# Optimization experiments

Hardware: AMD Instinct MI355X
Metric: run time of the kernel (lower is better)

Reference implementation:

```python
import jax, jax.numpy as jnp
import numpy as np

MODES = 32
WIDTH = 64


def crelu(z):
    # split-complex ReLU (torch.relu is undefined on complex; this is the standard fix)
    return jax.nn.relu(z.real) + 1j * jax.nn.relu(z.imag)


def _linear_params(key, fan_in, fan_out):
    k1, k2 = jax.random.split(key)
    s = 1.0 / np.sqrt(fan_in)
    W = jax.random.uniform(k1, (fan_out, fan_in), minval=-s, maxval=s, dtype=jnp.float32)
    b = jax.random.uniform(k2, (fan_out,), minval=-s, maxval=s, dtype=jnp.float32)
    return W, b


def setup_inputs() -> dict:
    key = jax.random.key(0)
    ks = jax.random.split(key, 8)
    B, G = 32768, 512
    H0, H1, H2 = 1024, 512, 64  # hidden_layers; H2 == WIDTH
    FD = 128                    # field_dim
    geometry_input = jax.random.normal(ks[0], (B, G), dtype=jnp.float32)
    W_in, b_in = _linear_params(ks[1], G, H0)
    W_h1, b_h1 = _linear_params(ks[2], H0, H1)
    W_h2, b_h2 = _linear_params(ks[3], H1, H2)
    w0 = jax.random.normal(ks[4], (MODES, WIDTH), dtype=jnp.float32)
    w1 = jax.random.normal(ks[5], (MODES, WIDTH), dtype=jnp.float32)
    lin1_W, lin1_b = _linear_params(ks[6], WIDTH, WIDTH)
    k7a, k7b = jax.random.split(ks[7])
    lin2_W, lin2_b = _linear_params(k7a, WIDTH, WIDTH)
    W_out, b_out = _linear_params(k7b, H2, FD)
    return dict(geometry_input=geometry_input, W_in=W_in, b_in=b_in,
                W_h1=W_h1, b_h1=b_h1, W_h2=W_h2, b_h2=b_h2,
                w0=w0, w1=w1, lin1_W=lin1_W, lin1_b=lin1_b,
                lin2_W=lin2_W, lin2_b=lin2_b, W_out=W_out, b_out=b_out)


def reference(geometry_input, W_in, b_in, W_h1, b_h1, W_h2, b_h2,
              w0, w1, lin1_W, lin1_b, lin2_W, lin2_b, W_out, b_out):
    # MLP encoder: [B, G] -> [B, 64]
    x = jax.nn.relu(geometry_input @ W_in.T + b_in)
    x = jax.nn.relu(x @ W_h1.T + b_h1)
    x = jax.nn.relu(x @ W_h2.T + b_h2)
    # FNO block
    xh = jnp.fft.fftn(x)  # fftn over ALL axes, as in torch code -> complex64 [B, 64]
    phase = jnp.exp(1j * 2.0 * jnp.pi * jnp.arange(MODES) / MODES).astype(jnp.complex64)
    y = xh[:, None, :] * w0  # per-mode lift: [B, MODES, WIDTH]
    y = crelu(y)
    y = y * phase[None, :, None]  # diagonal L mode-multiply
    y = jnp.einsum('bmw,mw->bw', y, w1.astype(y.dtype))  # collapse modes -> [B, WIDTH]
    y = crelu(y @ lin1_W.T + lin1_b)  # real weights on complex acts
    y = y @ lin2_W.T + lin2_b
    y = jnp.fft.ifftn(y)  # [B, 64] complex
    out = y @ W_out.T + b_out  # [B, field_dim] complex
    return out
```

## Files before the change

### kernel.cpp

```cpp
#include <hip/hip_runtime.h>
#include <hip/hip_bf16.h>


#define PI2F 6.28318530717958647692f

typedef __attribute__((ext_vector_type(8))) short short8;
typedef __attribute__((ext_vector_type(4))) float f32x4;

__device__ __forceinline__ unsigned short f2bf(float f) {
  unsigned int u = __float_as_uint(f);
  u += 0x7fff + ((u >> 16) & 1);
  return (unsigned short)(u >> 16);
}
__device__ __forceinline__ unsigned int pack_bf16x2(float a, float b) {
  return (unsigned int)f2bf(a) | ((unsigned int)f2bf(b) << 16);
}

__device__ __forceinline__ void gl2lds16(const void* gptr, const void* lptr) {
  __builtin_amdgcn_global_load_lds(
      (const __attribute__((address_space(1))) unsigned int*)(unsigned long long)gptr,
      (__attribute__((address_space(3))) unsigned int*)(unsigned int)(unsigned long long)lptr,
      16, 0, 0);
}

__global__ __launch_bounds__(256) void conv_all(
    const float* __restrict__ geom, const float* __restrict__ Win,
    const float* __restrict__ Wh1, const float* __restrict__ Wh2,
    unsigned short* __restrict__ dg, unsigned short* __restrict__ dw,
    unsigned short* __restrict__ d1, unsigned short* __restrict__ d2)
{
  int i = blockIdx.x * 256 + threadIdx.x;
  const float* s; unsigned short* d; int off;
  if (i < 4194304)      { s = geom; d = dg; off = i; }
  else if (i < 4325376) { s = Win;  d = dw; off = i - 4194304; }
  else if (i < 4456448) { s = Wh1;  d = d1; off = i - 4325376; }
  else if (i < 4464640) { s = Wh2;  d = d2; off = i - 4456448; }
  else return;
  float4 v = ((const float4*)s)[off];
  uint2 p;
  p.x = pack_bf16x2(v.x, v.y);
  p.y = pack_bf16x2(v.z, v.w);
  ((uint2*)d)[off] = p;
}

template<int NBLOG, typename OUT>
__global__ __launch_bounds__(512, 1) void gemm_pipe(
    const unsigned short* __restrict__ A, const unsigned short* __restrict__ Bw,
    const float* __restrict__ bias, OUT* __restrict__ C, int N, int K)
{
  constexpr int BM = 128, BN = 256, BK = 64;
  constexpr int ASZ = BM * BK;
  constexpr int BSZ = BN * BK;
  constexpr int BUF = ASZ + BSZ;
  __shared__ __align__(16) unsigned short lds[3 * BUF];

  const int nwg = gridDim.x;
  const int cpx = nwg >> 3;
  const int orig = blockIdx.x;
  const int wg = (orig & 7) * cpx + (orig >> 3);
  const int mb = wg >> NBLOG;
  const int nb = wg & ((1 << NBLOG) - 1);
  const size_t m0 = (size_t)mb * BM;
  const size_t n0 = (size_t)nb * BN;

  const int tid = threadIdx.x;
  const int lane = tid & 63;
  const int wv = tid >> 6;
  const int q = lane >> 4, lr = lane & 15;
  const int x7 = lr & 7;
  const int wm = (wv >> 2) * 64;
  const int wn = (wv & 3) * 64;
  f32x4 acc[4][4] = {};

  auto STAGE = [&](int r, int kk) {
    unsigned short* dA = lds + r * BUF;
    #pragma unroll
    for (int u = 0; u < 6; ++u) {
      int e = wv * 6 + u;
      int isA = (e < 16) ? 1 : 0;
      int e2 = isA ? e : e - 16;
      int pc = e2 * 64 + lane;
      int row = pc >> 3, col = pc & 7;
      int lc = col ^ (row & 7);
      const unsigned short* src = isA ? A : Bw;
      size_t rb = isA ? m0 : n0;
      unsigned short* dst = dA + (isA ? 0 : ASZ) + e2 * 512;
      gl2lds16(src + (rb + row) * (size_t)K + kk + lc * 8, dst);
    }
  };

  const int nt = K / BK;
  STAGE(0, 0);
  STAGE(1, BK);
  asm volatile("s_waitcnt vmcnt(6)" ::: "memory");
  __builtin_amdgcn_s_barrier();

  int r0 = 0;
  for (int t = 0; t < nt; ++t) {
    const unsigned short* sA = lds + r0 * BUF;
    const unsigned short* sB = sA + ASZ;
    const bool st = (t + 2) < nt;
    const int r2 = (r0 >= 1) ? (r0 - 1) : 2;
    const int kk2 = (t + 2) * BK;

    short8 af[4][2], bfr[4][2];
    #pragma unroll
    for (int i = 0; i < 4; ++i)
      #pragma unroll
      for (int t2 = 0; t2 < 2; ++t2)
        af[i][t2] = *(const short8*)(sA + (wm + i * 16 + lr) * 64 + (((t2 << 2) | q) ^ x7) * 8);
    #pragma unroll
    for (int j = 0; j < 4; ++j)
      #pragma unroll
      for (int t2 = 0; t2 < 2; ++t2)
        bfr[j][t2] = *(const short8*)(sB + (wn + j * 16 + lr) * 64 + (((t2 << 2) | q) ^ x7) * 8);
    if (st) STAGE(r2, kk2);
    __builtin_amdgcn_s_setprio(1);
    #pragma unroll
    for (int i = 0; i < 4; ++i)
      #pragma unroll
      for (int j = 0; j < 4; ++j)
        #pragma unroll
        for (int t2 = 0; t2 < 2; ++t2)
          acc[i][j] = __builtin_amdgcn_mfma_f32_16x16x32_bf16(af[i][t2], bfr[j][t2], acc[i][j], 0, 0, 0);
    __builtin_amdgcn_s_setprio(0);

    asm volatile("s_waitcnt lgkmcnt(0)" ::: "memory");
    if (st) { asm volatile("s_waitcnt vmcnt(6)" ::: "memory"); }
    else    { asm volatile("s_waitcnt vmcnt(0)" ::: "memory"); }
    __builtin_amdgcn_s_barrier();
    r0 = (r0 + 1 >= 3) ? 0 : r0 + 1;
  }

  #pragma unroll
  for (int i = 0; i < 4; ++i)
    #pragma unroll
    for (int j = 0; j < 4; ++j) {
      size_t col = n0 + wn + j * 16 + lr;
      float bv = bias[col];
      #pragma unroll
      for (int r = 0; r < 4; ++r) {
        size_t row = m0 + wm + i * 16 + q * 4 + r;
        float v = acc[i][j][r] + bv;
        v = v > 0.f ? v : 0.f;
        if (sizeof(OUT) == 2) ((unsigned short*)C)[row * N + col] = f2bf(v);
        else                  ((float*)C)[row * N + col] = v;
      }
    }
}

__global__ __launch_bounds__(256) void gemm3_dft(
    const unsigned short* __restrict__ A, const unsigned short* __restrict__ Bw,
    const float* __restrict__ bias, float2* __restrict__ S0, int K)
{
  constexpr int BM = 128, BN = 64, BK = 64;
  __shared__ __align__(16) unsigned short lA[BM * BK];
  __shared__ __align__(16) unsigned short lB[BN * BK];
  __shared__ __align__(16) float xt[128][68];
  __shared__ float2 tw[64];
  const int tid = threadIdx.x;
  const int lane = tid & 63;
  const int wv = tid >> 6;
  const int q = lane >> 4, lr = lane & 15;
  const int x7 = lr & 7;
  const int wm = (wv >> 1) * 64;
  const int wn = (wv & 1) * 32;
  const size_t m0 = (size_t)blockIdx.x * BM;
  f32x4 acc[4][2] = {};
  constexpr int A_PW = (BM * BK / 512) / 4;
  constexpr int B_PW = (BN * BK / 512) / 4;

  if (tid < 64) {
    float sn, cs; sincosf(-PI2F * (float)tid / 64.f, &sn, &cs);
    tw[tid] = make_float2(cs, sn);
  }

  for (int k0 = 0; k0 < K; k0 += BK) {
    __syncthreads();
    #pragma unroll
    for (int s = 0; s < A_PW; ++s) {
      int instr = wv * A_PW + s;
      int pc = instr * 64 + lane;
      int row = pc >> 3, col = pc & 7;
      int lc = col ^ (row & 7);
      gl2lds16(A + (m0 + row) * (size_t)K + k0 + lc * 8, lA + instr * 512);
    }
    #pragma unroll
    for (int s = 0; s < B_PW; ++s) {
      int instr = wv * B_PW + s;
      int pc = instr * 64 + lane;
      int row = pc >> 3, col = pc & 7;
      int lc = col ^ (row & 7);
      gl2lds16(Bw + (size_t)row * K + k0 + lc * 8, lB + instr * 512);
    }
    __syncthreads();
    #pragma unroll
    for (int t = 0; t < 2; ++t) {
      short8 af[4], bfr[2];
      #pragma unroll
      for (int i = 0; i < 4; ++i) {
        int r = wm + i * 16 + lr;
        af[i] = *(const short8*)(lA + r * 64 + (((t << 2) | q) ^ x7) * 8);
      }
      #pragma unroll
      for (int j = 0; j < 2; ++j) {
        int r = wn + j * 16 + lr;
        bfr[j] = *(const short8*)(lB + r * 64 + (((t << 2) | q) ^ x7) * 8);
      }
      #pragma unroll
      for (int i = 0; i < 4; ++i)
        #pragma unroll
        for (int j = 0; j < 2; ++j)
          acc[i][j] = __builtin_amdgcn_mfma_f32_16x16x32_bf16(af[i], bfr[j], acc[i][j], 0, 0, 0);
    }
  }

  __syncthreads();
  #pragma unroll
  for (int i = 0; i < 4; ++i)
    #pragma unroll
    for (int j = 0; j < 2; ++j) {
      int col = wn + j * 16 + lr;
      float bv = bias[col];
      #pragma unroll
      for (int r = 0; r < 4; ++r) {
        int rowl = wm + i * 16 + q * 4 + r;
        float v = acc[i][j][r] + bv;
        xt[rowl][col] = v > 0.f ? v : 0.f;
      }
    }
  __syncthreads();

  const int k = tid & 63, rg = tid >> 6;
  #pragma unroll 1
  for (int half = 0; half < 2; ++half) {
    const int rb = rg * 32 + half * 16;
    float2 dacc[16] = {};
    #pragma unroll 1
    for (int w4 = 0; w4 < 16; ++w4) {
      int w = 4 * w4;
      int kw = k * w;
      float2 t0 = tw[kw & 63];
      float2 t1 = tw[(kw + k) & 63];
      float2 t2 = tw[(kw + 2 * k) & 63];
      float2 t3 = tw[(kw + 3 * k) & 63];
      #pragma unroll
      for (int r = 0; r < 16; ++r) {
        float4 xv = *(const float4*)(&xt[rb + r][w]);
        dacc[r].x += xv.x * t0.x + xv.y * t1.x + xv.z * t2.x + xv.w * t3.x;
        dacc[r].y += xv.x * t0.y + xv.y * t1.y + xv.z * t2.y + xv.w * t3.y;
      }
    }
    #pragma unroll
    for (int r = 0; r < 16; ++r)
      S0[(m0 + rb + r) * 64 + k] = dacc[r];
  }
}

__global__ __launch_bounds__(256) void precompute(
    const float* __restrict__ w0, const float* __restrict__ w1,
    const float* __restrict__ l2W, const float* __restrict__ l2b,
    float2* __restrict__ Ap, float2* __restrict__ Am,
    float2* __restrict__ Qt, float2* __restrict__ b2c)
{
  const int t = threadIdx.x;
  const int blk = blockIdx.x;
  if (blk == 0) {
    if (t < 64) {
      float apx = 0, apy = 0, amx = 0, amy = 0;
      for (int m = 0; m < 32; ++m) {
        float s0 = w0[m * 64 + t];
        float cf = w1[m * 64 + t] * s0;
        float sn, cs; sincosf(PI2F * (float)m / 32.f, &sn, &cs);
        if (s0 > 0.f)      { apx += cs * cf; apy += sn * cf; }
        else if (s0 < 0.f) { amx += cs * cf; amy += sn * cf; }
      }
      Ap[t] = make_float2(apx, apy);
      Am[t] = make_float2(amx, amy);
      float bx = 0, by = 0;
      for (int k = 0; k < 64; ++k) {
        float sn, cs; sincosf(PI2F * (float)((t * k) & 63) / 64.f, &sn, &cs);
        float lb = l2b[k] * (1.f / 64.f);
        bx += cs * lb; by += sn * lb;
      }
      b2c[t] = make_float2(bx, by);
    }
  } else {
    int e = (blk - 1) * 256 + t;
    int j = e >> 6, w = e & 63;
    float qx = 0, qy = 0;
    for (int k = 0; k < 64; ++k) {
      float sn, cs; sincosf(PI2F * (float)((j * k) & 63) / 64.f, &sn, &cs);
      float lw = l2W[k * 64 + w] * (1.f / 64.f);
      qx += cs * lw; qy += sn * lw;
    }
    Qt[w * 64 + j] = make_float2(qx, qy);
  }
}

template<int SIGN>
__global__ __launch_bounds__(256) void fft_stage1(
    const float2* __restrict__ Xin, float2* __restrict__ T)
{
  __shared__ __align__(16) float2 tile[128 * 34];
  __shared__ float2 tw16s[16];
  const int blk = blockIdx.x;
  const int b2 = blk >> 1, wh = (blk & 1) * 32;
  const int t = threadIdx.x;
  #pragma unroll
  for (int it = 0; it < 8; ++it) {
    int idx = it * 256 + t;
    int b1 = idx >> 4, wi = (idx & 15) * 2;
    float4 v = *(const float4*)&Xin[((size_t)(b1 * 256 + b2)) * 64 + wh + wi];
    *(float4*)&tile[b1 * 34 + wi] = v;
  }
  if (t < 16) {
    float sn, cs; sincosf(SIGN * PI2F * (float)t / 16.f, &sn, &cs);
    tw16s[t] = make_float2(cs, sn);
  }
  __syncthreads();
  float2 twr[16];
  #pragma unroll
  for (int j = 0; j < 16; ++j) twr[j] = tw16s[j];

  {
    const int n2a = t >> 5, w = t & 31;
    float2 d[16];
    #pragma unroll
    for (int n1 = 0; n1 < 16; ++n1)
      d[n1] = tile[(8 * n1 + n2a) * 34 + w];
    float2 y[16];
    #pragma unroll
    for (int k = 0; k < 16; ++k) {
      float2 a = d[0];
      #pragma unroll
      for (int n1 = 1; n1 < 16; ++n1) {
        float2 tv = twr[(n1 * k) & 15];
        a.x += d[n1].x * tv.x - d[n1].y * tv.y;
        a.y += d[n1].x * tv.y + d[n1].y * tv.x;
      }
      y[k] = a;
    }
    float sstep, cstep;
    sincosf(SIGN * PI2F * (float)n2a / 128.f, &sstep, &cstep);
    float2 rot = make_float2(1.f, 0.f);
    #pragma unroll
    for (int k = 0; k < 16; ++k) {
      float2 a = y[k];
      y[k] = make_float2(a.x * rot.x - a.y * rot.y, a.x * rot.y + a.y * rot.x);
      float nrx = rot.x * cstep - rot.y * sstep;
      rot.y = rot.x * sstep + rot.y * cstep;
      rot.x = nrx;
    }
    __syncthreads();
    #pragma unroll
    for (int k = 0; k < 16; ++k)
      tile[(n2a * 16 + k) * 34 + w] = y[k];
  }
  __syncthreads();

  const int wB = t & 31, qB = t >> 5;
  float sstep, cstep;
  sincosf(SIGN * PI2F * (float)(16 * b2) / 32768.f, &sstep, &cstep);
  #pragma unroll
  for (int h = 0; h < 2; ++h) {
    const int k1p = qB + 8 * h;
    float2 d[8];
    #pragma unroll
    for (int n2 = 0; n2 < 8; ++n2)
      d[n2] = tile[(n2 * 16 + k1p) * 34 + wB];
    float2 acc[8];
    #pragma unroll
    for (int k2p = 0; k2p < 8; ++k2p) {
      float2 a = d[0];
      #pragma unroll
      for (int n2 = 1; n2 < 8; ++n2) {
        float2 tv = twr[(2 * n2 * k2p) & 15];
        a.x += d[n2].x * tv.x - d[n2].y * tv.y;
        a.y += d[n2].x * tv.y + d[n2].y * tv.x;
      }
      acc[k2p] = a;
    }
    float sb, cb;
    sincosf(SIGN * PI2F * (float)(b2 * k1p) / 32768.f, &sb, &cb);
    float2 rot = make_float2(cb, sb);
    #pragma unroll
    for (int k2p = 0; k2p < 8; ++k2p) {
      int k1 = k1p + 16 * k2p;
      float2 a = acc[k2p];
      T[((size_t)k1 * 256 + b2) * 64 + wh + wB] =
          make_float2(a.x * rot.x - a.y * rot.y, a.x * rot.y + a.y * rot.x);
      float nrx = rot.x * cstep - rot.y * sstep;
      rot.y = rot.x * sstep + rot.y * cstep;
      rot.x = nrx;
    }
  }
}

template<int SIGN, bool SCALE>
__global__ __launch_bounds__(256) void fft_stage2(
    const float2* __restrict__ T, float2* __restrict__ X)
{
  __shared__ __align__(16) float2 tile[256 * 18];
  __shared__ float2 tw16s[16];
  const int blk = blockIdx.x;
  const int k1 = blk >> 2, wq = (blk & 3) * 16;
  const int t = threadIdx.x;
  #pragma unroll
  for (int it = 0; it < 8; ++it) {
    int idx = it * 256 + t;
    int r2 = idx >> 3, wi = (idx & 7) * 2;
    float4 v = *(const float4*)&T[((size_t)k1 * 256 + r2) * 64 + wq + wi];
    *(float4*)&tile[r2 * 18 + wi] = v;
  }
  if (t < 16) {
    float sn, cs; sincosf(SIGN * PI2F * (float)t / 16.f, &sn, &cs);
    tw16s[t] = make_float2(cs, sn);
  }
  __syncthreads();
  float2 twr[16];
  #pragma unroll
  for (int j = 0; j < 16; ++j) twr[j] = tw16s[j];

  {
    const int n2a = t >> 4, w = t & 15;
    float2 d[16];
    #pragma unroll
    for (int n1 = 0; n1 < 16; ++n1)
      d[n1] = tile[(16 * n1 + n2a) * 18 + w];
    float2 y[16];
    #pragma unroll
    for (int k = 0; k < 16; ++k) {
      float2 a = d[0];
      #pragma unroll
      for (int n1 = 1; n1 < 16; ++n1) {
        float2 tv = twr[(n1 * k) & 15];
        a.x += d[n1].x * tv.x - d[n1].y * tv.y;
        a.y += d[n1].x * tv.y + d[n1].y * tv.x;
      }
      y[k] = a;
    }
    float sstep, cstep;
    sincosf(SIGN * PI2F * (float)n2a / 256.f, &sstep, &cstep);
    float2 rot = make_float2(1.f, 0.f);
    #pragma unroll
    for (int k = 0; k < 16; ++k) {
      float2 a = y[k];
      y[k] = make_float2(a.x * rot.x - a.y * rot.y, a.x * rot.y + a.y * rot.x);
      float nrx = rot.x * cstep - rot.y * sstep;
      rot.y = rot.x * sstep + rot.y * cstep;
      rot.x = nrx;
    }
    __syncthreads();
    #pragma unroll
    for (int k = 0; k < 16; ++k)
      tile[(n2a * 16 + k) * 18 + w] = y[k];
  }
  __syncthreads();

  const int k1pb = t >> 4, wB = t & 15;
  float2 d[16];
  #pragma unroll
  for (int n2 = 0; n2 < 16; ++n2)
    d[n2] = tile[(n2 * 16 + k1pb) * 18 + wB];
  const float sc = SCALE ? (1.f / 32768.f) : 1.f;
  #pragma unroll
  for (int k2p = 0; k2p < 16; ++k2p) {
    float2 a = d[0];
    #pragma unroll
    for (int n2 = 1; n2 < 16; ++n2) {
      float2 tv = twr[(n2 * k2p) & 15];
      a.x += d[n2].x * tv.x - d[n2].y * tv.y;
      a.y += d[n2].x * tv.y + d[n2].y * tv.x;
    }
    int k2 = k1pb + 16 * k2p;
    size_t row = (size_t)(k1 + 128 * k2);
    X[row * 64 + wq + wB] = make_float2(a.x * sc, a.y * sc);
  }
}

__global__ __launch_bounds__(256) void pw_lin(
    const float2* __restrict__ xh,
    const float2* __restrict__ Ap, const float2* __restrict__ Am,
    const float* __restrict__ l1W, const float* __restrict__ l1b,
    const float2* __restrict__ Qt, const float2* __restrict__ b2c,
    float2* __restrict__ u)
{
  __shared__ __align__(16) float2 tile[32][64];
  __shared__ __align__(16) float2 qt[64 * 64];
  const int t = threadIdx.x;
  const int lane = t & 63;
  const int wv = t >> 6;
  const size_t b0 = (size_t)blockIdx.x * 32;

  #pragma unroll
  for (int s = 0; s < 8; ++s) {
    int instr = wv * 8 + s;
    gl2lds16((const char*)Qt + instr * 1024 + lane * 16,
             (const char*)qt + instr * 1024);
  }

  for (int it = 0; it < 8; ++it) {
    int idx = it * 256 + t;
    int r = idx >> 6, w = idx & 63;
    float2 xv = xh[(b0 + r) * 64 + w];
    float2 Aa = (xv.x >= 0.f) ? Ap[w] : Am[w];
    float2 Ab = (xv.y >= 0.f) ? Ap[w] : Am[w];
    tile[r][w] = make_float2(xv.x * Aa.x - xv.y * Ab.y,
                             xv.x * Aa.y + xv.y * Ab.x);
  }
  __syncthreads();

  const int n = lane, rg = wv;

  {
    float2 acc[8] = {};
    const float* wrow = l1W + n * 64;
    float4 lwn = *(const float4*)wrow;
    #pragma unroll 1
    for (int w2 = 0; w2 < 16; ++w2) {
      float4 lw = lwn;
      lwn = *(const float4*)(wrow + 4 * ((w2 + 1) & 15));
      int w = 4 * w2;
      #pragma unroll
      for (int r = 0; r < 8; ++r) {
        const float4* rowp = (const float4*)(&tile[rg * 8 + r][w]);
        float4 y01 = rowp[0];
        float4 y23 = rowp[1];
        acc[r].x += y01.x * lw.x + y01.z * lw.y + y23.x * lw.z + y23.z * lw.w;
        acc[r].y += y01.y * lw.x + y01.w * lw.y + y23.y * lw.z + y23.w * lw.w;
      }
    }
    float bb = l1b[n];
    #pragma unroll
    for (int r = 0; r < 8; ++r) {
      float zr = acc[r].x + bb; zr = zr > 0.f ? zr : 0.f;
      float zi = acc[r].y;      zi = zi > 0.f ? zi : 0.f;
      tile[rg * 8 + r][n] = make_float2(zr, zi);
    }
  }

  {
    const int j = lane;
    float2 acc[8] = {};
    #pragma unroll 1
    for (int w2 = 0; w2 < 16; ++w2) {
      int w = 4 * w2;
      float2 q0 = qt[(w + 0) * 64 + j];
      float2 q1 = qt[(w + 1) * 64 + j];
      float2 q2 = qt[(w + 2) * 64 + j];
      float2 q3 = qt[(w + 3) * 64 + j];
      #pragma unroll
      for (int r = 0; r < 8; ++r) {
        const float4* rowp = (const float4*)(&tile[rg * 8 + r][w]);
        float4 z01 = rowp[0];
        float4 z23 = rowp[1];
        acc[r].x += z01.x * q0.x - z01.y * q0.y
                  + z01.z * q1.x - z01.w * q1.y
                  + z23.x * q2.x - z23.y * q2.y
                  + z23.z * q3.x - z23.w * q3.y;
        acc[r].y += z01.x * q0.y + z01.y * q0.x
                  + z01.z * q1.y + z01.w * q1.x
                  + z23.x * q2.y + z23.y * q2.x
                  + z23.z * q3.y + z23.w * q3.x;
      }
    }
    float2 bc = b2c[j];
    #pragma unroll
    for (int r = 0; r < 8; ++r)
      u[(b0 + rg * 8 + r) * 64 + j] = make_float2(acc[r].x + bc.x, acc[r].y + bc.y);
  }
}

template<int MODE>
__global__ __launch_bounds__(256) void final_out(
    const float2* __restrict__ v, const float* __restrict__ Wout,
    const float* __restrict__ bout, float* __restrict__ out)
{
  __shared__ __align__(16) float2 vt[32][64];
  const int t = threadIdx.x;
  const size_t b0 = (size_t)blockIdx.x * 32;
  for (int it = 0; it < 8; ++it) {
    int idx = it * 256 + t;
    int r = idx >> 6, w = idx & 63;
    vt[r][w] = v[(b0 + r) * 64 + w];
  }
  __syncthreads();
  const int f = t & 127, rg = t >> 7;
  const float* wrow = Wout + f * 64;
  float2 acc[16] = {};
  float2 wvn = *(const float2*)wrow;
  #pragma unroll 1
  for (int j2 = 0; j2 < 32; ++j2) {
    float2 wc = wvn;
    wvn = *(const float2*)(wrow + 2 * ((j2 + 1) & 31));
    #pragma unroll
    for (int r = 0; r < 16; ++r) {
      float4 vv = *(const float4*)(&vt[rg * 16 + r][2 * j2]);
      acc[r].x += vv.x * wc.x + vv.z * wc.y;
      acc[r].y += vv.y * wc.x + vv.w * wc.y;
    }
  }
  float bb = bout[f];
  #pragma unroll
  for (int r = 0; r < 16; ++r) {
    size_t idx = (b0 + rg * 16 + r) * 128 + f;
    if (MODE == 0) out[idx] = acc[r].x + bb;
    else ((float2*)out)[idx] = make_float2(acc[r].x + bb, acc[r].y);
  }
}

extern "C" void kernel_launch(void* const* d_in, const int* in_sizes, int n_in,
                              void* d_out, int out_size, void* d_ws, size_t ws_size,
                              hipStream_t stream)
{
  (void)in_sizes; (void)n_in; (void)ws_size;
  const float* geom = (const float*)d_in[0];
  const float* Win  = (const float*)d_in[1];
  const float* bin  = (const float*)d_in[2];
  const float* Wh1  = (const float*)d_in[3];
  const float* bh1  = (const float*)d_in[4];
  const float* Wh2  = (const float*)d_in[5];
  const float* bh2  = (const float*)d_in[6];
  const float* w0   = (const float*)d_in[7];
  const float* w1   = (const float*)d_in[8];
  const float* l1W  = (const float*)d_in[9];
  const float* l1b  = (const float*)d_in[10];
  const float* l2W  = (const float*)d_in[11];
  const float* l2b  = (const float*)d_in[12];
  const float* Wout = (const float*)d_in[13];
  const float* bout = (const float*)d_in[14];

  char* ws = (char*)d_ws;
  const size_t MB = 1048576ull;
  unsigned short* geomb = (unsigned short*)(ws);
  unsigned short* x2b   = (unsigned short*)(ws);
  unsigned short* x1b   = (unsigned short*)(ws + 32 * MB);
  float2* S0  = (float2*)(ws + 40 * MB);
  float2* S1  = (float2*)(ws + 56 * MB);
  float2* Ap  = (float2*)(ws + 72 * MB);
  float2* Am  = (float2*)(ws + 72 * MB + 512);
  float2* b2c = (float2*)(ws + 72 * MB + 1024);
  float2* Qt  = (float2*)(ws + 72 * MB + 1536);
  unsigned short* Winb = (unsigned short*)(ws + 96 * MB);
  unsigned short* Wh1b = (unsigned short*)(ws + 97 * MB);
  unsigned short* Wh2b = (unsigned short*)(ws + 98 * MB);

  conv_all<<<17441, 256, 0, stream>>>(geom, Win, Wh1, Wh2,
                                      geomb, Winb, Wh1b, Wh2b);

  gemm_pipe<2, unsigned short><<<1024, 512, 0, stream>>>(
      geomb, Winb, bin, x1b, 1024, 512);
  gemm_pipe<1, unsigned short><<<512, 512, 0, stream>>>(
      x1b, Wh1b, bh1, x2b, 512, 1024);
  gemm3_dft<<<256, 256, 0, stream>>>(x2b, Wh2b, bh2, S0, 512);

  precompute<<<17, 256, 0, stream>>>(w0, w1, l2W, l2b, Ap, Am, Qt, b2c);
  fft_stage1<-1><<<512, 256, 0, stream>>>(S0, S1);
  fft_stage2<-1, false><<<512, 256, 0, stream>>>(S1, S0);
  pw_lin<<<1024, 256, 0, stream>>>(S0, Ap, Am, l1W, l1b, Qt, b2c, S1);
  fft_stage1<1><<<512, 256, 0, stream>>>(S1, S0);
  fft_stage2<1, true><<<512, 256, 0, stream>>>(S0, S1);
  if (out_size >= 8388608) {
    final_out<1><<<1024, 256, 0, stream>>>(S1, Wout, bout, (float*)d_out);
  } else {
    final_out<0><<<1024, 256, 0, stream>>>(S1, Wout, bout, (float*)d_out);
  }
}
```

Measured before the change: 413.1 us.

## Split FFT stage DFTs across more threads and load tiles via global_load_lds

Both FFT stage kernels now split each 16-point DFT's outputs across two thread groups, which halves per-thread register arrays and raises the thread count. Stage 1 uses 1024 narrower blocks and stage 2 uses 512-thread blocks. Global-to-LDS staging now uses direct global_load_lds 16-byte transfers into unpadded tiles, replacing register round trips. The cost is more recomputed twiddle setup and possible LDS bank conflicts now that the tile padding is gone.

```diff
diff --git a/kernel.cpp b/kernel.cpp
--- a/kernel.cpp
+++ b/kernel.cpp
@@ -21,6 +21,23 @@
       (const __attribute__((address_space(1))) unsigned int*)(unsigned long long)gptr,
       (__attribute__((address_space(3))) unsigned int*)(unsigned int)(unsigned long long)lptr,
       16, 0, 0);
+}
+
+template<int K0>
+__device__ __forceinline__ void dft16part(const float2* d, const float2* twr,
+                                          float2* y)
+{
+  #pragma unroll
+  for (int kk = 0; kk < 8; ++kk) {
+    float2 a = d[0];
+    #pragma unroll
+    for (int n1 = 1; n1 < 16; ++n1) {
+      float2 tv = twr[(n1 * (K0 + kk)) & 15];
+      a.x += d[n1].x * tv.x - d[n1].y * tv.y;
+      a.y += d[n1].x * tv.y + d[n1].y * tv.x;
+    }
+    y[kk] = a;
+  }
 }
 
 __global__ __launch_bounds__(256) void conv_all(
@@ -302,17 +319,19 @@
 __global__ __launch_bounds__(256) void fft_stage1(
     const float2* __restrict__ Xin, float2* __restrict__ T)
 {
-  __shared__ __align__(16) float2 tile[128 * 34];
+  __shared__ __align__(16) float2 tile[128 * 16];
   __shared__ float2 tw16s[16];
   const int blk = blockIdx.x;
-  const int b2 = blk >> 1, wh = (blk & 1) * 32;
+  const int b2 = blk >> 2, wh = (blk & 3) * 16;
   const int t = threadIdx.x;
-  #pragma unroll
-  for (int it = 0; it < 8; ++it) {
-    int idx = it * 256 + t;
-    int b1 = idx >> 4, wi = (idx & 15) * 2;
-    float4 v = *(const float4*)&Xin[((size_t)(b1 * 256 + b2)) * 64 + wh + wi];
-    *(float4*)&tile[b1 * 34 + wi] = v;
+  const int lane = t & 63, wvv = t >> 6;
+  #pragma unroll
+  for (int s = 0; s < 4; ++s) {
+    int instr = wvv * 4 + s;
+    int b1 = instr * 8 + (lane >> 3);
+    int wi = (lane & 7) * 2;
+    gl2lds16(Xin + ((size_t)(b1 * 256 + b2)) * 64 + wh + wi,
+             (const char*)tile + instr * 1024);
   }
   if (t < 16) {
     float sn, cs; sincosf(SIGN * PI2F * (float)t / 16.f, &sn, &cs);
@@ -323,95 +342,87 @@
   #pragma unroll
   for (int j = 0; j < 16; ++j) twr[j] = tw16s[j];
 
+  const int ko = t >> 7;
+  const int n2a = (t >> 4) & 7, w = t & 15;
+  float2 y[8];
   {
-    const int n2a = t >> 5, w = t & 31;
     float2 d[16];
     #pragma unroll
     for (int n1 = 0; n1 < 16; ++n1)
-      d[n1] = tile[(8 * n1 + n2a) * 34 + w];
-    float2 y[16];
-    #pragma unroll
-    for (int k = 0; k < 16; ++k) {
-      float2 a = d[0];
-      #pragma unroll
-      for (int n1 = 1; n1 < 16; ++n1) {
-        float2 tv = twr[(n1 * k) & 15];
-        a.x += d[n1].x * tv.x - d[n1].y * tv.y;
-        a.y += d[n1].x * tv.y + d[n1].y * tv.x;
-      }
-      y[k] = a;
-    }
+      d[n1] = tile[(8 * n1 + n2a) * 16 + w];
+    if (ko == 0) dft16part<0>(d, twr, y);
+    else         dft16part<8>(d, twr, y);
     float sstep, cstep;
     sincosf(SIGN * PI2F * (float)n2a / 128.f, &sstep, &cstep);
-    float2 rot = make_float2(1.f, 0.f);
-    #pragma unroll
-    for (int k = 0; k < 16; ++k) {
-      float2 a = y[k];
-      y[k] = make_float2(a.x * rot.x - a.y * rot.y, a.x * rot.y + a.y * rot.x);
+    float s0, c0;
+    sincosf(SIGN * PI2F * (float)(n2a * (ko * 8)) / 128.f, &s0, &c0);
+    float2 rot = make_float2(c0, s0);
+    #pragma unroll
+    for (int kk = 0; kk < 8; ++kk) {
+      float2 a = y[kk];
+      y[kk] = make_float2(a.x * rot.x - a.y * rot.y, a.x * rot.y + a.y * rot.x);
       float nrx = rot.x * cstep - rot.y * sstep;
       rot.y = rot.x * sstep + rot.y * cstep;
       rot.x = nrx;
     }
-    __syncthreads();
-    #pragma unroll
-    for (int k = 0; k < 16; ++k)
-      tile[(n2a * 16 + k) * 34 + w] = y[k];
-  }
-  __syncthreads();
-
-  const int wB = t & 31, qB = t >> 5;
+  }
+  __syncthreads();
+  #pragma unroll
+  for (int kk = 0; kk < 8; ++kk)
+    tile[(n2a * 16 + ko * 8 + kk) * 16 + w] = y[kk];
+  __syncthreads();
+
+  const int k1p = t >> 4, wB = t & 15;
+  float2 d2[8];
+  #pragma unroll
+  for (int n2 = 0; n2 < 8; ++n2)
+    d2[n2] = tile[(n2 * 16 + k1p) * 16 + wB];
+  float2 acc[8];
+  #pragma unroll
+  for (int k2p = 0; k2p < 8; ++k2p) {
+    float2 a = d2[0];
+    #pragma unroll
+    for (int n2 = 1; n2 < 8; ++n2) {
+      float2 tv = twr[(2 * n2 * k2p) & 15];
+      a.x += d2[n2].x * tv.x - d2[n2].y * tv.y;
+      a.y += d2[n2].x * tv.y + d2[n2].y * tv.x;
+    }
+    acc[k2p] = a;
+  }
   float sstep, cstep;
   sincosf(SIGN * PI2F * (float)(16 * b2) / 32768.f, &sstep, &cstep);
-  #pragma unroll
-  for (int h = 0; h < 2; ++h) {
-    const int k1p = qB + 8 * h;
-    float2 d[8];
-    #pragma unroll
-    for (int n2 = 0; n2 < 8; ++n2)
-      d[n2] = tile[(n2 * 16 + k1p) * 34 + wB];
-    float2 acc[8];
-    #pragma unroll
-    for (int k2p = 0; k2p < 8; ++k2p) {
-      float2 a = d[0];
-      #pragma unroll
-      for (int n2 = 1; n2 < 8; ++n2) {
-        float2 tv = twr[(2 * n2 * k2p) & 15];
-        a.x += d[n2].x * tv.x - d[n2].y * tv.y;
-        a.y += d[n2].x * tv.y + d[n2].y * tv.x;
-      }
-      acc[k2p] = a;
-    }
-    float sb, cb;
-    sincosf(SIGN * PI2F * (float)(b2 * k1p) / 32768.f, &sb, &cb);
-    float2 rot = make_float2(cb, sb);
-    #pragma unroll
-    for (int k2p = 0; k2p < 8; ++k2p) {
-      int k1 = k1p + 16 * k2p;
-      float2 a = acc[k2p];
-      T[((size_t)k1 * 256 + b2) * 64 + wh + wB] =
-          make_float2(a.x * rot.x - a.y * rot.y, a.x * rot.y + a.y * rot.x);
-      float nrx = rot.x * cstep - rot.y * sstep;
-      rot.y = rot.x * sstep + rot.y * cstep;
-      rot.x = nrx;
-    }
+  float sb, cb;
+  sincosf(SIGN * PI2F * (float)(b2 * k1p) / 32768.f, &sb, &cb);
+  float2 rot = make_float2(cb, sb);
+  #pragma unroll
+  for (int k2p = 0; k2p < 8; ++k2p) {
+    int k1 = k1p + 16 * k2p;
+    float2 a = acc[k2p];
+    T[((size_t)k1 * 256 + b2) * 64 + wh + wB] =
+        make_float2(a.x * rot.x - a.y * rot.y, a.x * rot.y + a.y * rot.x);
+    float nrx = rot.x * cstep - rot.y * sstep;
+    rot.y = rot.x * sstep + rot.y * cstep;
+    rot.x = nrx;
   }
 }
 
 template<int SIGN, bool SCALE>
-__global__ __launch_bounds__(256) void fft_stage2(
+__global__ __launch_bounds__(512) void fft_stage2(
     const float2* __restrict__ T, float2* __restrict__ X)
 {
-  __shared__ __align__(16) float2 tile[256 * 18];
+  __shared__ __align__(16) float2 tile[256 * 16];
   __shared__ float2 tw16s[16];
   const int blk = blockIdx.x;
   const int k1 = blk >> 2, wq = (blk & 3) * 16;
   const int t = threadIdx.x;
-  #pragma unroll
-  for (int it = 0; it < 8; ++it) {
-    int idx = it * 256 + t;
-    int r2 = idx >> 3, wi = (idx & 7) * 2;
-    float4 v = *(const float4*)&T[((size_t)k1 * 256 + r2) * 64 + wq + wi];
-    *(float4*)&tile[r2 * 18 + wi] = v;
+  const int lane = t & 63, wvv = t >> 6;
+  #pragma unroll
+  for (int s = 0; s < 4; ++s) {
+    int instr = wvv * 4 + s;
+    int r2 = instr * 8 + (lane >> 3);
+    int wi = (lane & 7) * 2;
+    gl2lds16(T + ((size_t)k1 * 256 + r2) * 64 + wq + wi,
+             (const char*)tile + instr * 1024);
   }
   if (t < 16) {
     float sn, cs; sincosf(SIGN * PI2F * (float)t / 16.f, &sn, &cs);
@@ -422,60 +433,52 @@
   #pragma unroll
   for (int j = 0; j < 16; ++j) twr[j] = tw16s[j];
 
+  const int ko = t >> 8;
+  const int n2a = (t >> 4) & 15, w = t & 15;
+  float2 y[8];
   {
-    const int n2a = t >> 4, w = t & 15;
     float2 d[16];
     #pragma unroll
     for (int n1 = 0; n1 < 16; ++n1)
-      d[n1] = tile[(16 * n1 + n2a) * 18 + w];
-    float2 y[16];
-    #pragma unroll
-    for (int k = 0; k < 16; ++k) {
-      float2 a = d[0];
-      #pragma unroll
-      for (int n1 = 1; n1 < 16; ++n1) {
-        float2 tv = twr[(n1 * k) & 15];
-        a.x += d[n1].x * tv.x - d[n1].y * tv.y;
-        a.y += d[n1].x * tv.y + d[n1].y * tv.x;
-      }
-      y[k] = a;
-    }
+      d[n1] = tile[(16 * n1 + n2a) * 16 + w];
+    if (ko == 0) dft16part<0>(d, twr, y);
+    else         dft16part<8>(d, twr, y);
     float sstep, cstep;
     sincosf(SIGN * PI2F * (float)n2a / 256.f, &sstep, &cstep);
-    float2 rot = make_float2(1.f, 0.f);
-    #pragma unroll
-    for (int k = 0; k < 16; ++k) {
-      float2 a = y[k];
-      y[k] = make_float2(a.x * rot.x - a.y * rot.y, a.x * rot.y + a.y * rot.x);
+    float s0, c0;
+    sincosf(SIGN * PI2F * (float)(n2a * (ko * 8)) / 256.f, &s0, &c0);
+    float2 rot = make_float2(c0, s0);
+    #pragma unroll
+    for (int kk = 0; kk < 8; ++kk) {
+      float2 a = y[kk];
+      y[kk] = make_float2(a.x * rot.x - a.y * rot.y, a.x * rot.y + a.y * rot.x);
       float nrx = rot.x * cstep - rot.y * sstep;
       rot.y = rot.x * sstep + rot.y * cstep;
       rot.x = nrx;
     }
-    __syncthreads();
-    #pragma unroll
-    for (int k = 0; k < 16; ++k)
-      tile[(n2a * 16 + k) * 18 + w] = y[k];
-  }
-  __syncthreads();
-
-  const int k1pb = t >> 4, wB = t & 15;
-  float2 d[16];
+  }
+  __syncthreads();
+  #pragma unroll
+  for (int kk = 0; kk < 8; ++kk)
+    tile[(n2a * 16 + ko * 8 + kk) * 16 + w] = y[kk];
+  __syncthreads();
+
+  const int kb = t >> 8;
+  const int k1pb = (t >> 4) & 15, wB = t & 15;
+  float2 d2[16];
   #pragma unroll
   for (int n2 = 0; n2 < 16; ++n2)
-    d[n2] = tile[(n2 * 16 + k1pb) * 18 + wB];
+    d2[n2] = tile[(n2 * 16 + k1pb) * 16 + wB];
+  float2 acc[8];
+  if (kb == 0) dft16part<0>(d2, twr, acc);
+  else         dft16part<8>(d2, twr, acc);
   const float sc = SCALE ? (1.f / 32768.f) : 1.f;
   #pragma unroll
-  for (int k2p = 0; k2p < 16; ++k2p) {
-    float2 a = d[0];
-    #pragma unroll
-    for (int n2 = 1; n2 < 16; ++n2) {
-      float2 tv = twr[(n2 * k2p) & 15];
-      a.x += d[n2].x * tv.x - d[n2].y * tv.y;
-      a.y += d[n2].x * tv.y + d[n2].y * tv.x;
-    }
+  for (int kk = 0; kk < 8; ++kk) {
+    int k2p = kb * 8 + kk;
     int k2 = k1pb + 16 * k2p;
     size_t row = (size_t)(k1 + 128 * k2);
-    X[row * 64 + wq + wB] = make_float2(a.x * sc, a.y * sc);
+    X[row * 64 + wq + wB] = make_float2(acc[kk].x * sc, acc[kk].y * sc);
   }
 }
 
@@ -656,11 +659,11 @@
   gemm3_dft<<<256, 256, 0, stream>>>(x2b, Wh2b, bh2, S0, 512);
 
   precompute<<<17, 256, 0, stream>>>(w0, w1, l2W, l2b, Ap, Am, Qt, b2c);
-  fft_stage1<-1><<<512, 256, 0, stream>>>(S0, S1);
-  fft_stage2<-1, false><<<512, 256, 0, stream>>>(S1, S0);
+  fft_stage1<-1><<<1024, 256, 0, stream>>>(S0, S1);
+  fft_stage2<-1, false><<<512, 512, 0, stream>>>(S1, S0);
   pw_lin<<<1024, 256, 0, stream>>>(S0, Ap, Am, l1W, l1b, Qt, b2c, S1);
-  fft_stage1<1><<<512, 256, 0, stream>>>(S1, S0);
-  fft_stage2<1, true><<<512, 256, 0, stream>>>(S0, S1);
+  fft_stage1<1><<<1024, 256, 0, stream>>>(S1, S0);
+  fft_stage2<1, true><<<512, 512, 0, stream>>>(S0, S1);
   if (out_size >= 8388608) {
     final_out<1><<<1024, 256, 0, stream>>>(S1, Wout, bout, (float*)d_out);
   } else {
```

Measured after the change: 405.9 us. About the same (-1.7%).
